# Performance work log

Hardware: AMD Instinct MI355X
Metric: run time of the kernel (lower is better)

Reference implementation:

```python
import jax, jax.numpy as jnp
import numpy as np

S, B, D, H = 1024, 8, 768, 12
PROMPT_NUM = 8
DH = D // H


def setup_inputs() -> dict:
    key = jax.random.key(0)
    ks = jax.random.split(key, 5)
    scale = 1.0 / np.sqrt(D)
    return {
        "x": jax.random.normal(ks[0], (S, B, D), dtype=jnp.float32),
        "in_proj_weight": jax.random.normal(ks[1], (3 * D, D), dtype=jnp.float32) * scale,
        "in_proj_bias": jax.random.normal(ks[2], (3 * D,), dtype=jnp.float32) * 0.02,
        "out_w": jax.random.normal(ks[3], (D, D), dtype=jnp.float32) * scale,
        "out_b": jax.random.normal(ks[4], (D,), dtype=jnp.float32) * 0.02,
    }


def reference(x, in_proj_weight, in_proj_bias, out_w, out_b):
    # x: (S, B, D) -> (B, S, D)
    xt = jnp.transpose(x, (1, 0, 2))
    qkv = xt @ in_proj_weight.T + in_proj_bias  # (B, S, 3D)
    q, k, v = jnp.split(qkv, 3, axis=-1)
    q = q.reshape(B, S, H, DH)
    k = k.reshape(B, S, H, DH)
    v = v.reshape(B, S, H, DH)
    # affinity (n, q, k, h); scale by sqrt(head_dim)
    aff = jnp.einsum("nqhc,nkhc->nqkh", q / np.sqrt(DH), k)
    # prompt masking: CLS_MASK | PROMPT_MASK
    tokens = S - PROMPT_NUM
    m = np.zeros((S, S), dtype=bool)
    m[0, tokens:] = True          # CLS_MASK: CLS query can't attend to prompts
    m[tokens:, tokens:] = True    # PROMPT_MASK: prompts can't attend to prompts
    m = jnp.asarray(m)
    aff = jnp.where(m[None, :, :, None], jnp.float32(-10000.0), aff)
    # softmax over key axis (dim=-2 of nqkh)
    aff = jax.nn.softmax(aff, axis=2)
    mix = jnp.einsum("nqlh,nlhc->nqhc", aff, v)  # (B, S, H, DH)
    out = mix.reshape(B, S, D) @ out_w.T + out_b
    # transpose back to (S, B, ...)
    return (
        jnp.transpose(q, (1, 0, 2, 3)),
        jnp.transpose(k, (1, 0, 2, 3)),
        jnp.transpose(v, (1, 0, 2, 3)),
        jnp.transpose(out, (1, 0, 2)),
    )
```

## Files before the change

kernel.cpp:

```cpp
#include <hip/hip_runtime.h>


typedef unsigned short u16;
typedef __attribute__((ext_vector_type(8))) short short8;
typedef __attribute__((ext_vector_type(4))) short short4v;
typedef __attribute__((ext_vector_type(4))) float floatx4;
typedef __attribute__((ext_vector_type(4))) unsigned short ushort4v;

#define NB 8
#define NS 1024
#define NH 12
#define ND 768
#define DHD 64
#define TOKENS 1016
#define QKV_OUT_STRIDE 6291456

#if __has_builtin(__builtin_amdgcn_exp2f)
#define EXP2(x) __builtin_amdgcn_exp2f(x)
#else
#define EXP2(x) exp2f(x)
#endif

#if defined(__HIP_DEVICE_COMPILE__)
  #if __has_builtin(__builtin_amdgcn_mfma_f32_16x16x16bf16_1k)
    #define MFMA16(a, b, c) __builtin_amdgcn_mfma_f32_16x16x16bf16_1k(a, b, c, 0, 0, 0)
  #else
    #define MFMA16(a, b, c) __builtin_amdgcn_mfma_f32_16x16x16_bf16(a, b, c, 0, 0, 0)
  #endif
  #define GLD16(g, l)                                                        \
    __builtin_amdgcn_global_load_lds(                                        \
        (const __attribute__((address_space(1))) void*)(g),                  \
        (__attribute__((address_space(3))) void*)(l), 16, 0, 0)
#else
  #define MFMA16(a, b, c) (c)
  #define GLD16(g, l) ((void)0)
#endif

__device__ __forceinline__ u16 f2bf(float f) {
  union { float f; unsigned u; } c; c.f = f;
  return (u16)((c.u + 0x7fffu + ((c.u >> 16) & 1u)) >> 16);
}

#define CVT_B0 6144
#define CVT_B1 1728
#define CVT_B2 576
__global__ __launch_bounds__(256) void cvt3(
    const float* __restrict__ s0, u16* __restrict__ d0,
    const float* __restrict__ s1, u16* __restrict__ d1,
    const float* __restrict__ s2, u16* __restrict__ d2) {
  int blk = blockIdx.x;
  const float* s; u16* d;
  if (blk < CVT_B0) { s = s0; d = d0; }
  else if (blk < CVT_B0 + CVT_B1) { s = s1; d = d1; blk -= CVT_B0; }
  else { s = s2; d = d2; blk -= CVT_B0 + CVT_B1; }
  const int i = (blk * 256 + (int)threadIdx.x) * 4;
  const float4 v = *(const float4*)(s + i);
  ushort4v o;
  o.x = f2bf(v.x); o.y = f2bf(v.y); o.z = f2bf(v.z); o.w = f2bf(v.w);
  *(ushort4v*)(d + i) = o;
}

__global__ __launch_bounds__(256) void qkv_gemm(
    const u16* __restrict__ Xb, const u16* __restrict__ Wb,
    const float* __restrict__ bias, float* __restrict__ out) {
  __shared__ __align__(16) u16 As[128][32];
  __shared__ __align__(16) u16 Bs[128][32];
  const int tid = threadIdx.x;
  const int lane = tid & 63, wave = tid >> 6;
  const int l15 = lane & 15, quad = lane >> 4;
  const int wm = wave & 1, wn = wave >> 1;
  const int mblk = blockIdx.x * 128;
  const int nblk = blockIdx.y * 128;

  floatx4 acc[4][4];
#pragma unroll
  for (int i = 0; i < 4; ++i)
#pragma unroll
    for (int j = 0; j < 4; ++j) acc[i][j] = (floatx4)0.f;

  const int lr = lane >> 2;
  const int lc = (lane & 3) * 8;
  const int c0 = wave * 2;
  const int r0 = c0 * 16 + lr, r1 = r0 + 16;
  const int gm0 = mblk + r0, gm1 = mblk + r1;
  const u16* ga0 = Xb + ((gm0 & 1023) * NB + (gm0 >> 10)) * ND + lc;
  const u16* ga1 = Xb + ((gm1 & 1023) * NB + (gm1 >> 10)) * ND + lc;
  const u16* gb0 = Wb + (nblk + r0) * ND + lc;
  const u16* gb1 = Wb + (nblk + r1) * ND + lc;
  u16* la0 = &As[c0 * 16][0];
  u16* la1 = &As[c0 * 16 + 16][0];
  u16* lb0 = &Bs[c0 * 16][0];
  u16* lb1 = &Bs[c0 * 16 + 16][0];

  for (int kt = 0; kt < 24; ++kt) {
    const int k0 = kt * 32;
    GLD16(ga0 + k0, la0);
    GLD16(ga1 + k0, la1);
    GLD16(gb0 + k0, lb0);
    GLD16(gb1 + k0, lb1);
    __syncthreads();
    short8 af[4], bfr[4];
#pragma unroll
    for (int mt = 0; mt < 4; ++mt)
      af[mt] = *(const short8*)&As[wm * 64 + mt * 16 + l15][quad * 8];
#pragma unroll
    for (int nt = 0; nt < 4; ++nt)
      bfr[nt] = *(const short8*)&Bs[wn * 64 + nt * 16 + l15][quad * 8];
#pragma unroll
    for (int mt = 0; mt < 4; ++mt)
#pragma unroll
      for (int nt = 0; nt < 4; ++nt)
        acc[mt][nt] = __builtin_amdgcn_mfma_f32_16x16x32_bf16(
            af[mt], bfr[nt], acc[mt][nt], 0, 0, 0);
    __syncthreads();
  }

#pragma unroll
  for (int mt = 0; mt < 4; ++mt) {
#pragma unroll
    for (int r = 0; r < 4; ++r) {
      const int gm = mblk + wm * 64 + mt * 16 + quad * 4 + r;
      const int b = gm >> 10, s = gm & 1023;
#pragma unroll
      for (int nt = 0; nt < 4; ++nt) {
        const int gn = nblk + wn * 64 + nt * 16 + l15;
        const int seg = gn / ND;
        const int nn = gn - seg * ND;
        out[seg * QKV_OUT_STRIDE + (s * NB + b) * ND + nn] = acc[mt][nt][r] + bias[gn];
      }
    }
  }
}

__global__ __launch_bounds__(256) void prep(
    const float* __restrict__ K, const float* __restrict__ V,
    u16* __restrict__ Kb, u16* __restrict__ Vt) {
  __shared__ u16 tile[DHD][40];
  const int t = threadIdx.x;
  const int bh = blockIdx.y;
  const int b = bh / NH, h = bh % NH;
  const int s0 = blockIdx.x * 32;
  const int sl = t >> 3;
  const int c0 = (t & 7) * 8;
  const int s = s0 + sl;
  if (blockIdx.z == 0) {
    const float* src = K + ((s * NB + b) * NH + h) * DHD + c0;
    const float4 v0 = *(const float4*)src;
    const float4 v1 = *(const float4*)(src + 4);
    short8 o;
    o[0] = f2bf(v0.x); o[1] = f2bf(v0.y); o[2] = f2bf(v0.z); o[3] = f2bf(v0.w);
    o[4] = f2bf(v1.x); o[5] = f2bf(v1.y); o[6] = f2bf(v1.z); o[7] = f2bf(v1.w);
    *(short8*)(Kb + ((size_t)bh * NS + s) * DHD + c0) = o;
  } else {
    const float* src = V + ((s * NB + b) * NH + h) * DHD + c0;
    const float4 v0 = *(const float4*)src;
    const float4 v1 = *(const float4*)(src + 4);
    tile[c0 + 0][sl] = f2bf(v0.x); tile[c0 + 1][sl] = f2bf(v0.y);
    tile[c0 + 2][sl] = f2bf(v0.z); tile[c0 + 3][sl] = f2bf(v0.w);
    tile[c0 + 4][sl] = f2bf(v1.x); tile[c0 + 5][sl] = f2bf(v1.y);
    tile[c0 + 6][sl] = f2bf(v1.z); tile[c0 + 7][sl] = f2bf(v1.w);
    __syncthreads();
    const int c = t >> 2;
    const int so = (t & 3) * 8;
    *(short8*)(Vt + ((size_t)bh * DHD + c) * NS + s0 + so) =
        *(const short8*)&tile[c][so];
  }
}

__global__ __launch_bounds__(256) void attn(
    const float* __restrict__ Q, const u16* __restrict__ Kb,
    const u16* __restrict__ Vt, u16* __restrict__ mix) {
  __shared__ __align__(16) u16 Kt[64][72];
  __shared__ __align__(16) u16 Vs[64][72];
  const int tid = threadIdx.x;
  const int lane = tid & 63, wave = tid >> 6;
  const int l15 = lane & 15, quad = lane >> 4;
  const int bh = blockIdx.y;
  const int b = bh / NH, h = bh % NH;
  const int qb = blockIdx.x * 128 + wave * 32;

  short8 qf[2][2];
  bool qmask[2];
#pragma unroll
  for (int j = 0; j < 2; ++j) {
    const int qj = qb + j * 16 + l15;
    qmask[j] = (qj == 0 || qj >= TOKENS);
    const float* qp = Q + ((qj * NB + b) * NH + h) * DHD + quad * 8;
#pragma unroll
    for (int e = 0; e < 8; ++e) {
      qf[j][0][e] = (short)f2bf(qp[e]);
      qf[j][1][e] = (short)f2bf(qp[32 + e]);
    }
  }

  floatx4 O[2][4];
#pragma unroll
  for (int j = 0; j < 2; ++j)
#pragma unroll
    for (int g = 0; g < 4; ++g) O[j][g] = (floatx4)0.f;
  float li[2] = {0.f, 0.f};

  const u16* kg = Kb + (size_t)bh * NS * DHD;
  const u16* vg = Vt + (size_t)bh * DHD * NS;

  const float C1 = 0.125f * 1.44269504089f;
  const float C0 = -10.0f * 1.44269504089f;

  const int srow = tid >> 2;
  const int scol = (tid & 3) * 16;

  short8 pk0, pk1, pv0, pv1;
  {
    pk0 = *(const short8*)(kg + srow * DHD + scol);
    pk1 = *(const short8*)(kg + srow * DHD + scol + 8);
    pv0 = *(const short8*)(vg + srow * NS + scol);
    pv1 = *(const short8*)(vg + srow * NS + scol + 8);
  }

  for (int it = 0; it < 16; ++it) {
    *(short8*)&Kt[srow][scol] = pk0;
    *(short8*)&Kt[srow][scol + 8] = pk1;
    *(short8*)&Vs[srow][scol] = pv0;
    *(short8*)&Vs[srow][scol + 8] = pv1;
    __syncthreads();
    if (it < 15) {
      const int k0 = (it + 1) * 64;
      pk0 = *(const short8*)(kg + (k0 + srow) * DHD + scol);
      pk1 = *(const short8*)(kg + (k0 + srow) * DHD + scol + 8);
      pv0 = *(const short8*)(vg + srow * NS + k0 + scol);
      pv1 = *(const short8*)(vg + srow * NS + k0 + scol + 8);
    }
    const bool mrow = (it == 15) && (quad >= 2);
#pragma unroll
    for (int sub = 0; sub < 4; ++sub) {
      const short8 kf0 = *(const short8*)&Kt[sub * 16 + l15][quad * 8];
      const short8 kf1 = *(const short8*)&Kt[sub * 16 + l15][32 + quad * 8];
      short4v pb[2];
#pragma unroll
      for (int j = 0; j < 2; ++j) {
        floatx4 a = (floatx4)0.f;
        a = __builtin_amdgcn_mfma_f32_16x16x32_bf16(kf0, qf[j][0], a, 0, 0, 0);
        a = __builtin_amdgcn_mfma_f32_16x16x32_bf16(kf1, qf[j][1], a, 0, 0, 0);
        float p[4];
#pragma unroll
        for (int r = 0; r < 4; ++r) p[r] = EXP2(fmaf(a[r], C1, C0));
        if (sub == 3 && mrow && qmask[j]) {
#pragma unroll
          for (int r = 0; r < 4; ++r) p[r] = 0.f;
        }
        li[j] += (p[0] + p[1]) + (p[2] + p[3]);
#pragma unroll
        for (int r = 0; r < 4; ++r) pb[j][r] = (short)f2bf(p[r]);
      }
#pragma unroll
      for (int g = 0; g < 4; ++g) {
        const short4v vf = *(const short4v*)&Vs[g * 16 + l15][sub * 16 + quad * 4];
        O[0][g] = MFMA16(vf, pb[0], O[0][g]);
        O[1][g] = MFMA16(vf, pb[1], O[1][g]);
      }
    }
    __syncthreads();
  }

#pragma unroll
  for (int j = 0; j < 2; ++j) {
    float l = li[j];
    l += __shfl_xor(l, 16);
    l += __shfl_xor(l, 32);
    const float rl = 1.0f / l;
    const int qj = qb + j * 16 + l15;
    u16* mp = mix + ((size_t)b * NS + qj) * ND + h * DHD + quad * 4;
#pragma unroll
    for (int g = 0; g < 4; ++g) {
      ushort4v o;
#pragma unroll
      for (int r = 0; r < 4; ++r) o[r] = f2bf(O[j][g][r] * rl);
      *(ushort4v*)(mp + g * 16) = o;
    }
  }
}

__global__ __launch_bounds__(256) void out_gemm(
    const u16* __restrict__ A, const u16* __restrict__ Wb,
    const float* __restrict__ bias, float* __restrict__ out) {
  __shared__ __align__(16) u16 As[128][32];
  __shared__ __align__(16) u16 Bs[128][32];
  const int tid = threadIdx.x;
  const int lane = tid & 63, wave = tid >> 6;
  const int l15 = lane & 15, quad = lane >> 4;
  const int wm = wave & 1, wn = wave >> 1;
  const int mblk = blockIdx.x * 128;
  const int nblk = blockIdx.y * 128;

  floatx4 acc[4][4];
#pragma unroll
  for (int i = 0; i < 4; ++i)
#pragma unroll
    for (int j = 0; j < 4; ++j) acc[i][j] = (floatx4)0.f;

  const int lr = lane >> 2;
  const int lc = (lane & 3) * 8;
  const int c0 = wave * 2;
  const int r0 = c0 * 16 + lr, r1 = r0 + 16;
  const u16* ga0 = A + (mblk + r0) * ND + lc;
  const u16* ga1 = A + (mblk + r1) * ND + lc;
  const u16* gb0 = Wb + (nblk + r0) * ND + lc;
  const u16* gb1 = Wb + (nblk + r1) * ND + lc;
  u16* la0 = &As[c0 * 16][0];
  u16* la1 = &As[c0 * 16 + 16][0];
  u16* lb0 = &Bs[c0 * 16][0];
  u16* lb1 = &Bs[c0 * 16 + 16][0];

  for (int kt = 0; kt < 24; ++kt) {
    const int k0 = kt * 32;
    GLD16(ga0 + k0, la0);
    GLD16(ga1 + k0, la1);
    GLD16(gb0 + k0, lb0);
    GLD16(gb1 + k0, lb1);
    __syncthreads();
    short8 af[4], bfr[4];
#pragma unroll
    for (int mt = 0; mt < 4; ++mt)
      af[mt] = *(const short8*)&As[wm * 64 + mt * 16 + l15][quad * 8];
#pragma unroll
    for (int nt = 0; nt < 4; ++nt)
      bfr[nt] = *(const short8*)&Bs[wn * 64 + nt * 16 + l15][quad * 8];
#pragma unroll
    for (int mt = 0; mt < 4; ++mt)
#pragma unroll
      for (int nt = 0; nt < 4; ++nt)
        acc[mt][nt] = __builtin_amdgcn_mfma_f32_16x16x32_bf16(
            af[mt], bfr[nt], acc[mt][nt], 0, 0, 0);
    __syncthreads();
  }

#pragma unroll
  for (int mt = 0; mt < 4; ++mt) {
#pragma unroll
    for (int r = 0; r < 4; ++r) {
      const int gm = mblk + wm * 64 + mt * 16 + quad * 4 + r;
      const int b = gm >> 10, s = gm & 1023;
#pragma unroll
      for (int nt = 0; nt < 4; ++nt) {
        const int gn = nblk + wn * 64 + nt * 16 + l15;
        out[(s * NB + b) * ND + gn] = acc[mt][nt][r] + bias[gn];
      }
    }
  }
}

extern "C" void kernel_launch(void* const* d_in, const int* in_sizes, int n_in,
                              void* d_out, int out_size, void* d_ws, size_t ws_size,
                              hipStream_t stream) {
  const float* X  = (const float*)d_in[0];
  const float* W  = (const float*)d_in[1];
  const float* Bi = (const float*)d_in[2];
  const float* Ow = (const float*)d_in[3];
  const float* Ob = (const float*)d_in[4];
  float* out = (float*)d_out;

  u16* Xb  = (u16*)d_ws;
  u16* Wb  = Xb  + 6291456;
  u16* Owb = Wb  + 1769472;
  u16* Vt  = Owb + 589824;
  u16* Kb  = Vt  + 6291456;
  u16* mix = Kb  + 6291456;

  cvt3<<<CVT_B0 + CVT_B1 + CVT_B2, 256, 0, stream>>>(X, Xb, W, Wb, Ow, Owb);
  qkv_gemm<<<dim3(64, 18), 256, 0, stream>>>(Xb, Wb, Bi, out);
  prep<<<dim3(32, 96, 2), 256, 0, stream>>>(out + QKV_OUT_STRIDE,
                                            out + 2 * QKV_OUT_STRIDE, Kb, Vt);
  attn<<<dim3(8, 96), 256, 0, stream>>>(out, Kb, Vt, mix);
  out_gemm<<<dim3(64, 6), 256, 0, stream>>>(mix, Owb, Ob, out + 3 * QKV_OUT_STRIDE);
}
```

Baseline: 244.7 us.

## Double K-step per barrier in GEMMs, remap attention blocks per XCD, pack bf16 converts

Both GEMM kernels now load two 32-wide K slices into separate LDS buffers per iteration, halving the number of loop trips and barrier pairs (12 instead of 24). The attention kernel remaps its linear block index so that consecutive blocks on the same XCD share a batch-head, aiming for better L2 reuse of K/V. It also replaces the scalar bf16 conversion of probabilities with paired conversion intrinsics. Using more LDS per block may reduce occupancy, and the remap assumes a specific grid shape.

```diff
diff --git a/kernel.cpp b/kernel.cpp
--- a/kernel.cpp
+++ b/kernel.cpp
@@ -1,4 +1,5 @@
 #include <hip/hip_runtime.h>
+#include <hip/hip_bf16.h>
 
 
 typedef unsigned short u16;
@@ -6,6 +7,7 @@
 typedef __attribute__((ext_vector_type(4))) short short4v;
 typedef __attribute__((ext_vector_type(4))) float floatx4;
 typedef __attribute__((ext_vector_type(4))) unsigned short ushort4v;
+typedef __attribute__((ext_vector_type(2))) unsigned int uint2v;
 
 #define NB 8
 #define NS 1024
@@ -63,8 +65,10 @@
 __global__ __launch_bounds__(256) void qkv_gemm(
     const u16* __restrict__ Xb, const u16* __restrict__ Wb,
     const float* __restrict__ bias, float* __restrict__ out) {
-  __shared__ __align__(16) u16 As[128][32];
-  __shared__ __align__(16) u16 Bs[128][32];
+  __shared__ __align__(16) u16 As0[128][32];
+  __shared__ __align__(16) u16 As1[128][32];
+  __shared__ __align__(16) u16 Bs0[128][32];
+  __shared__ __align__(16) u16 Bs1[128][32];
   const int tid = threadIdx.x;
   const int lane = tid & 63, wave = tid >> 6;
   const int l15 = lane & 15, quad = lane >> 4;
@@ -87,31 +91,46 @@
   const u16* ga1 = Xb + ((gm1 & 1023) * NB + (gm1 >> 10)) * ND + lc;
   const u16* gb0 = Wb + (nblk + r0) * ND + lc;
   const u16* gb1 = Wb + (nblk + r1) * ND + lc;
-  u16* la0 = &As[c0 * 16][0];
-  u16* la1 = &As[c0 * 16 + 16][0];
-  u16* lb0 = &Bs[c0 * 16][0];
-  u16* lb1 = &Bs[c0 * 16 + 16][0];
-
-  for (int kt = 0; kt < 24; ++kt) {
-    const int k0 = kt * 32;
-    GLD16(ga0 + k0, la0);
-    GLD16(ga1 + k0, la1);
-    GLD16(gb0 + k0, lb0);
-    GLD16(gb1 + k0, lb1);
-    __syncthreads();
-    short8 af[4], bfr[4];
+  u16* lA00 = &As0[c0 * 16][0];
+  u16* lA10 = &As0[c0 * 16 + 16][0];
+  u16* lA01 = &As1[c0 * 16][0];
+  u16* lA11 = &As1[c0 * 16 + 16][0];
+  u16* lB00 = &Bs0[c0 * 16][0];
+  u16* lB10 = &Bs0[c0 * 16 + 16][0];
+  u16* lB01 = &Bs1[c0 * 16][0];
+  u16* lB11 = &Bs1[c0 * 16 + 16][0];
+
+  for (int kt = 0; kt < 12; ++kt) {
+    const int k0 = kt * 64;
+    GLD16(ga0 + k0, lA00);
+    GLD16(ga0 + k0 + 32, lA01);
+    GLD16(ga1 + k0, lA10);
+    GLD16(ga1 + k0 + 32, lA11);
+    GLD16(gb0 + k0, lB00);
+    GLD16(gb0 + k0 + 32, lB01);
+    GLD16(gb1 + k0, lB10);
+    GLD16(gb1 + k0 + 32, lB11);
+    __syncthreads();
+    short8 af0[4], af1[4], bf0[4], bf1[4];
+#pragma unroll
+    for (int mt = 0; mt < 4; ++mt) {
+      af0[mt] = *(const short8*)&As0[wm * 64 + mt * 16 + l15][quad * 8];
+      af1[mt] = *(const short8*)&As1[wm * 64 + mt * 16 + l15][quad * 8];
+    }
+#pragma unroll
+    for (int nt = 0; nt < 4; ++nt) {
+      bf0[nt] = *(const short8*)&Bs0[wn * 64 + nt * 16 + l15][quad * 8];
+      bf1[nt] = *(const short8*)&Bs1[wn * 64 + nt * 16 + l15][quad * 8];
+    }
 #pragma unroll
     for (int mt = 0; mt < 4; ++mt)
-      af[mt] = *(const short8*)&As[wm * 64 + mt * 16 + l15][quad * 8];
-#pragma unroll
-    for (int nt = 0; nt < 4; ++nt)
-      bfr[nt] = *(const short8*)&Bs[wn * 64 + nt * 16 + l15][quad * 8];
-#pragma unroll
-    for (int mt = 0; mt < 4; ++mt)
-#pragma unroll
-      for (int nt = 0; nt < 4; ++nt)
+#pragma unroll
+      for (int nt = 0; nt < 4; ++nt) {
         acc[mt][nt] = __builtin_amdgcn_mfma_f32_16x16x32_bf16(
-            af[mt], bfr[nt], acc[mt][nt], 0, 0, 0);
+            af0[mt], bf0[nt], acc[mt][nt], 0, 0, 0);
+        acc[mt][nt] = __builtin_amdgcn_mfma_f32_16x16x32_bf16(
+            af1[mt], bf1[nt], acc[mt][nt], 0, 0, 0);
+      }
     __syncthreads();
   }
 
@@ -175,9 +194,12 @@
   const int tid = threadIdx.x;
   const int lane = tid & 63, wave = tid >> 6;
   const int l15 = lane & 15, quad = lane >> 4;
-  const int bh = blockIdx.y;
+  const int L = (int)blockIdx.x + 8 * (int)blockIdx.y;
+  const int xcd = L & 7, tt = L >> 3;
+  const int bh = xcd + 8 * (tt >> 3);
+  const int qx = tt & 7;
   const int b = bh / NH, h = bh % NH;
-  const int qb = blockIdx.x * 128 + wave * 32;
+  const int qb = qx * 128 + wave * 32;
 
   short8 qf[2][2];
   bool qmask[2];
@@ -249,8 +271,12 @@
           for (int r = 0; r < 4; ++r) p[r] = 0.f;
         }
         li[j] += (p[0] + p[1]) + (p[2] + p[3]);
-#pragma unroll
-        for (int r = 0; r < 4; ++r) pb[j][r] = (short)f2bf(p[r]);
+        __hip_bfloat162 w0 = __float22bfloat162_rn(make_float2(p[0], p[1]));
+        __hip_bfloat162 w1 = __float22bfloat162_rn(make_float2(p[2], p[3]));
+        uint2v pw;
+        pw.x = *(const unsigned*)&w0;
+        pw.y = *(const unsigned*)&w1;
+        pb[j] = __builtin_bit_cast(short4v, pw);
       }
 #pragma unroll
       for (int g = 0; g < 4; ++g) {
@@ -283,8 +309,10 @@
 __global__ __launch_bounds__(256) void out_gemm(
     const u16* __restrict__ A, const u16* __restrict__ Wb,
     const float* __restrict__ bias, float* __restrict__ out) {
-  __shared__ __align__(16) u16 As[128][32];
-  __shared__ __align__(16) u16 Bs[128][32];
+  __shared__ __align__(16) u16 As0[128][32];
+  __shared__ __align__(16) u16 As1[128][32];
+  __shared__ __align__(16) u16 Bs0[128][32];
+  __shared__ __align__(16) u16 Bs1[128][32];
   const int tid = threadIdx.x;
   const int lane = tid & 63, wave = tid >> 6;
   const int l15 = lane & 15, quad = lane >> 4;
@@ -306,31 +334,46 @@
   const u16* ga1 = A + (mblk + r1) * ND + lc;
   const u16* gb0 = Wb + (nblk + r0) * ND + lc;
   const u16* gb1 = Wb + (nblk + r1) * ND + lc;
-  u16* la0 = &As[c0 * 16][0];
-  u16* la1 = &As[c0 * 16 + 16][0];
-  u16* lb0 = &Bs[c0 * 16][0];
-  u16* lb1 = &Bs[c0 * 16 + 16][0];
-
-  for (int kt = 0; kt < 24; ++kt) {
-    const int k0 = kt * 32;
-    GLD16(ga0 + k0, la0);
-    GLD16(ga1 + k0, la1);
-    GLD16(gb0 + k0, lb0);
-    GLD16(gb1 + k0, lb1);
-    __syncthreads();
-    short8 af[4], bfr[4];
+  u16* lA00 = &As0[c0 * 16][0];
+  u16* lA10 = &As0[c0 * 16 + 16][0];
+  u16* lA01 = &As1[c0 * 16][0];
+  u16* lA11 = &As1[c0 * 16 + 16][0];
+  u16* lB00 = &Bs0[c0 * 16][0];
+  u16* lB10 = &Bs0[c0 * 16 + 16][0];
+  u16* lB01 = &Bs1[c0 * 16][0];
+  u16* lB11 = &Bs1[c0 * 16 + 16][0];
+
+  for (int kt = 0; kt < 12; ++kt) {
+    const int k0 = kt * 64;
+    GLD16(ga0 + k0, lA00);
+    GLD16(ga0 + k0 + 32, lA01);
+    GLD16(ga1 + k0, lA10);
+    GLD16(ga1 + k0 + 32, lA11);
+    GLD16(gb0 + k0, lB00);
+    GLD16(gb0 + k0 + 32, lB01);
+    GLD16(gb1 + k0, lB10);
+    GLD16(gb1 + k0 + 32, lB11);
+    __syncthreads();
+    short8 af0[4], af1[4], bf0[4], bf1[4];
+#pragma unroll
+    for (int mt = 0; mt < 4; ++mt) {
+      af0[mt] = *(const short8*)&As0[wm * 64 + mt * 16 + l15][quad * 8];
+      af1[mt] = *(const short8*)&As1[wm * 64 + mt * 16 + l15][quad * 8];
+    }
+#pragma unroll
+    for (int nt = 0; nt < 4; ++nt) {
+      bf0[nt] = *(const short8*)&Bs0[wn * 64 + nt * 16 + l15][quad * 8];
+      bf1[nt] = *(const short8*)&Bs1[wn * 64 + nt * 16 + l15][quad * 8];
+    }
 #pragma unroll
     for (int mt = 0; mt < 4; ++mt)
-      af[mt] = *(const short8*)&As[wm * 64 + mt * 16 + l15][quad * 8];
-#pragma unroll
-    for (int nt = 0; nt < 4; ++nt)
-      bfr[nt] = *(const short8*)&Bs[wn * 64 + nt * 16 + l15][quad * 8];
-#pragma unroll
-    for (int mt = 0; mt < 4; ++mt)
-#pragma unroll
-      for (int nt = 0; nt < 4; ++nt)
+#pragma unroll
+      for (int nt = 0; nt < 4; ++nt) {
         acc[mt][nt] = __builtin_amdgcn_mfma_f32_16x16x32_bf16(
-            af[mt], bfr[nt], acc[mt][nt], 0, 0, 0);
+            af0[mt], bf0[nt], acc[mt][nt], 0, 0, 0);
+        acc[mt][nt] = __builtin_amdgcn_mfma_f32_16x16x32_bf16(
+            af1[mt], bf1[nt], acc[mt][nt], 0, 0, 0);
+      }
     __syncthreads();
   }
 
```

Result: no change. 245.7 us (+0.4%).
